# Kernel optimization log

Measured on AMD Instinct MI355X. Metric: run time of the kernel, lower is better.

## Reference

```python
import jax, jax.numpy as jnp
import numpy as np

EPS = 1e-3        # Memory.eps distance threshold
MOMENTUM = 0.999  # Memory.momentum
N, F, M = 500000, 256, 1024


def setup_inputs() -> dict:
    key = jax.random.key(0)
    k1, k2, k3, k4, k5 = jax.random.split(key, 5)
    return {
        "points": jax.random.normal(k1, (M, 3), dtype=jnp.float32),
        "descriptors": jax.random.normal(k2, (M, F), dtype=jnp.float32),
        # learned/stateful memory bank (params/buffers of the module)
        "mem_points": jax.random.normal(k3, (N, 3), dtype=jnp.float32),
        "mem_descriptors": jax.random.normal(k4, (N, F), dtype=jnp.float32),
        "usage": jax.random.randint(k5, (N,), 0, 1000, dtype=jnp.int32),
    }


def _moving(x, m):
    # faithful to Memory.moving: x*m + (1-m)*x  (== x, kept as written)
    return x * m + (1.0 - m) * x


def reference(points, descriptors, mem_points, mem_descriptors, usage):
    # ---- point_address: cdist (p=2) + argmin nearest neighbor ----
    # squared-distance expansion; [M, N] matrix
    d2 = (jnp.sum(points * points, axis=-1)[:, None]
          + jnp.sum(mem_points * mem_points, axis=-1)[None, :]
          - 2.0 * points @ mem_points.T)
    dist = jnp.sqrt(jnp.maximum(d2, 1e-12))
    dmin = jnp.min(dist, axis=-1)
    idx = jnp.argmin(dist, axis=-1)            # [M]
    mask = dmin > EPS                          # queries with no near match

    # ---- topk eviction: lowest-usage slots, assigned in query order ----
    # torch: idx[mask] = usage.topk(k=mask.sum(), largest=False).indices
    # static-shape equivalent: take top-M least-used, select first cumsum(mask)
    _, evict = jax.lax.top_k(-usage, points.shape[0])  # [M] least-used slots
    rank = jnp.cumsum(mask.astype(jnp.int32)) - 1      # position among masked
    idx = jnp.where(mask, evict[rank], idx)

    momentum = jnp.where(mask, 0.0, MOMENTUM)[:, None]  # [M, 1]

    # ---- write: usage bump + momentum scatter-update ----
    usage_new = usage.at[idx].add(1)
    pts_new = mem_points.at[idx].set(_moving(mem_points[idx], momentum))
    desc_new = mem_descriptors.at[idx].set(_moving(mem_descriptors[idx], momentum))

    out = jnp.concatenate([pts_new, desc_new], axis=1)  # [N, 3+F]
    return out, usage_new, idx
```

## Files before the change

### kernel.cpp

```cpp
#include <hip/hip_runtime.h>

#define N_TOT   500000
#define M_Q     1024
#define QB      16
#define NSPLIT  16
#define CAND_MAX 8192

#define ARGMIN_BLKS 1024
#define HIST_BLKS   32
#define USAGE_BLKS  64
#define CROWS       16
#define COPY_BLKS   (N_TOT / CROWS)
#define MEGA_BLKS   (ARGMIN_BLKS + HIST_BLKS + USAGE_BLKS + COPY_BLKS)
#define HIST_CHUNK  (N_TOT / HIST_BLKS)

static const unsigned OUT_ROWS  = 259u * (unsigned)N_TOT;
static const unsigned OUT_USAGE = OUT_ROWS;
static const unsigned OUT_IDX   = OUT_ROWS + (unsigned)N_TOT;

#define WS_PARTKEY 0
#define WS_PARTIDX 65536
#define WS_HISTP   131072
#define WS_V       262144
#define WS_CNT     262148
#define WS_KEYS    262152

__global__ __launch_bounds__(256) void k_mega(
    const float* __restrict__ pts,  const float* __restrict__ mpts,
    const float* __restrict__ mdesc, const int* __restrict__ usage,
    float* __restrict__ out,
    float* __restrict__ partKey, int* __restrict__ partIdx,
    int* __restrict__ histPart)
{
    __shared__ float smem[CROWS * 259];
    const int b   = blockIdx.x;
    const int tid = threadIdx.x;

    if (b < ARGMIN_BLKS) {
        const int qb = b & 63;
        const int ns = b >> 6;
        const int qbase = qb * QB;
        const int chunk = N_TOT / NSPLIT;
        const int n0 = ns * chunk;
        const int n1 = n0 + chunk;

        float* qs = smem;
        float* wk = smem + 64;
        int*   wi = (int*)(smem + 192);
        if (tid < QB * 3) qs[tid] = pts[qbase * 3 + tid];
        __syncthreads();

        float qx[QB], qy[QB], qz[QB];
#pragma unroll
        for (int i = 0; i < QB; i++) { qx[i] = qs[3*i]; qy[i] = qs[3*i+1]; qz[i] = qs[3*i+2]; }

        float bk[QB]; int bi[QB];
#pragma unroll
        for (int i = 0; i < QB; i++) { bk[i] = INFINITY; bi[i] = 0x7fffffff; }

        for (int n = n0 + tid; n < n1; n += 256) {
            float x = mpts[3*n+0], y = mpts[3*n+1], z = mpts[3*n+2];
            float h = 0.5f * (x*x + y*y + z*z);
#pragma unroll
            for (int i = 0; i < QB; i++) {
                float key = h - x*qx[i] - y*qy[i] - z*qz[i];
                bool lt = key < bk[i];
                bk[i] = lt ? key : bk[i];
                bi[i] = lt ? n   : bi[i];
            }
        }

        const int lane = tid & 63;
        const int wv   = tid >> 6;
#pragma unroll
        for (int off = 32; off > 0; off >>= 1) {
#pragma unroll
            for (int i = 0; i < QB; i++) {
                float ok = __shfl_down(bk[i], off, 64);
                int   oi = __shfl_down(bi[i], off, 64);
                if (ok < bk[i] || (ok == bk[i] && oi < bi[i])) { bk[i] = ok; bi[i] = oi; }
            }
        }
        if (lane == 0) {
#pragma unroll
            for (int i = 0; i < QB; i++) { wk[wv*QB + i] = bk[i]; wi[wv*QB + i] = bi[i]; }
        }
        __syncthreads();
        if (tid < QB) {
            float k = wk[tid]; int ix = wi[tid];
#pragma unroll
            for (int w = 1; w < 4; w++) {
                float ok = wk[w*QB + tid]; int oi = wi[w*QB + tid];
                if (ok < k || (ok == k && oi < ix)) { k = ok; ix = oi; }
            }
            partKey[(qbase + tid) * NSPLIT + ns] = k;
            partIdx[(qbase + tid) * NSPLIT + ns] = ix;
        }
    } else if (b < ARGMIN_BLKS + HIST_BLKS) {
        const int hb = b - ARGMIN_BLKS;
        const int r0 = hb * HIST_CHUNK;
        const int r1 = r0 + HIST_CHUNK;
        int* lh = (int*)smem;
#pragma unroll
        for (int i = 0; i < 4; i++) lh[tid + i * 256] = 0;
        __syncthreads();
        for (int n = r0 + tid; n < r1; n += 256) {
            unsigned v = (unsigned)usage[n];
            if (v > 1023u) v = 1023u;
            atomicAdd(&lh[v], 1);
        }
        __syncthreads();
#pragma unroll
        for (int i = 0; i < 4; i++) {
            int bin = tid + i * 256;
            histPart[hb * 1024 + bin] = lh[bin];
        }
    } else if (b < ARGMIN_BLKS + HIST_BLKS + USAGE_BLKS) {
        const int ub = b - ARGMIN_BLKS - HIST_BLKS;
        const int4* u4 = (const int4*)usage;
        float4* o4 = (float4*)(out + OUT_USAGE);
        const int TOT4 = N_TOT / 4;
        for (int g = ub * 256 + tid; g < TOT4; g += USAGE_BLKS * 256) {
            int4 u = u4[g];
            o4[g] = make_float4((float)u.x, (float)u.y, (float)u.z, (float)u.w);
        }
    } else {
        const int cb = b - (ARGMIN_BLKS + HIST_BLKS + USAGE_BLKS);
        const int n0 = cb * CROWS;
        const float4* src = (const float4*)(mdesc + (size_t)n0 * 256);
#pragma unroll
        for (int it = 0; it < 4; it++) {
            int g = tid + it * 256;
            float4 v = src[g];
            int e = g * 4;
            int r = e >> 8;
            int c = e & 255;
            float* d = smem + r * 259 + 3 + c;
            d[0] = v.x; d[1] = v.y; d[2] = v.z; d[3] = v.w;
        }
        if (tid < CROWS * 3) {
            int r = tid / 3, c = tid - r * 3;
            smem[r * 259 + c] = mpts[(size_t)n0 * 3 + tid];
        }
        __syncthreads();
        float4* dst4 = (float4*)(out + (size_t)cb * (CROWS * 259));
        const float4* s4 = (const float4*)smem;
#pragma unroll
        for (int it = 0; it < 5; it++) {
            int g = tid + it * 256;
            if (g < CROWS * 259 / 4) dst4[g] = s4[g];
        }
    }
}

__global__ __launch_bounds__(1024) void k_scanV(
    const int* __restrict__ histPart, int* __restrict__ Vout, int* __restrict__ cnt)
{
    __shared__ int scan[1024];
    const int t = threadIdx.x;
    int h = 0;
#pragma unroll
    for (int b = 0; b < HIST_BLKS; b++) h += histPart[b * 1024 + t];
    scan[t] = h; __syncthreads();
    for (int off = 1; off < 1024; off <<= 1) {
        int add = (t >= off) ? scan[t - off] : 0;
        __syncthreads();
        scan[t] += add;
        __syncthreads();
    }
    int cum  = scan[t] - h;
    int cumN = scan[t];
    if (cum < M_Q && cumN >= M_Q) { *Vout = t; *cnt = 0; }
}

__global__ __launch_bounds__(256) void k_collect(
    const int* __restrict__ usage, const int* __restrict__ Vp,
    int* __restrict__ cnt, unsigned* __restrict__ keys)
{
    const int V = *Vp;
    const int stride = gridDim.x * 256;
    for (int n = blockIdx.x * 256 + threadIdx.x; n < N_TOT; n += stride) {
        int u = usage[n];
        if (u <= V) {
            int p = atomicAdd(cnt, 1);
            if (p < CAND_MAX) keys[p] = ((unsigned)u << 19) | (unsigned)n;
        }
    }
}

__global__ __launch_bounds__(1024) void k_final(
    const float* __restrict__ pts,
    const float* __restrict__ partKey, const int* __restrict__ partIdx,
    const int* __restrict__ cntP, const unsigned* __restrict__ keysG,
    float* __restrict__ out)
{
    __shared__ unsigned keys[CAND_MAX];
    __shared__ int      mscan[1024];
    const int t = threadIdx.x;

    float bk = INFINITY; int bi = 0x7fffffff;
#pragma unroll
    for (int s = 0; s < NSPLIT; s++) {
        float k = partKey[t * NSPLIT + s];
        int   i = partIdx[t * NSPLIT + s];
        if (k < bk) { bk = k; bi = i; }
    }
    float px = pts[3*t], py = pts[3*t+1], pz = pts[3*t+2];
    float d2 = px*px + py*py + pz*pz + 2.0f * bk;
    const bool mask = d2 > 1e-6f;

    int C = *cntP; if (C > CAND_MAX) C = CAND_MAX;
    int P2 = 1; while (P2 < C) P2 <<= 1;
    for (int p = t; p < P2; p += 1024) keys[p] = (p < C) ? keysG[p] : 0xFFFFFFFFu;
    __syncthreads();

    for (int k = 2; k <= P2; k <<= 1) {
        for (int j = k >> 1; j > 0; j >>= 1) {
            for (int i = t; i < P2; i += 1024) {
                int ixj = i ^ j;
                if (ixj > i) {
                    unsigned a = keys[i], bb = keys[ixj];
                    bool up = ((i & k) == 0);
                    if ((a > bb) == up) { keys[i] = bb; keys[ixj] = a; }
                }
            }
            __syncthreads();
        }
    }

    mscan[t] = mask ? 1 : 0; __syncthreads();
    for (int off = 1; off < 1024; off <<= 1) {
        int add = (t >= off) ? mscan[t - off] : 0;
        __syncthreads();
        mscan[t] += add;
        __syncthreads();
    }
    int rank = mscan[t] - 1;
    int idx = mask ? (int)(keys[rank] & 0x7FFFFu) : bi;
    out[(size_t)OUT_IDX + (size_t)t] = (float)idx;
    atomicAdd(out + OUT_USAGE + idx, 1.0f);
}

extern "C" void kernel_launch(void* const* d_in, const int* in_sizes, int n_in,
                              void* d_out, int out_size, void* d_ws, size_t ws_size,
                              hipStream_t stream)
{
    (void)in_sizes; (void)n_in; (void)out_size; (void)ws_size;
    const float* pts   = (const float*)d_in[0];
    const float* mpts  = (const float*)d_in[2];
    const float* mdesc = (const float*)d_in[3];
    const int*   usage = (const int*)d_in[4];
    float* out = (float*)d_out;

    char* ws = (char*)d_ws;
    float*    partKey  = (float*)(ws + WS_PARTKEY);
    int*      partIdx  = (int*)(ws + WS_PARTIDX);
    int*      histPart = (int*)(ws + WS_HISTP);
    int*      Vp       = (int*)(ws + WS_V);
    int*      cnt      = (int*)(ws + WS_CNT);
    unsigned* keys     = (unsigned*)(ws + WS_KEYS);

    k_mega<<<MEGA_BLKS, 256, 0, stream>>>(pts, mpts, mdesc, usage, out,
                                          partKey, partIdx, histPart);
    k_scanV<<<1, 1024, 0, stream>>>(histPart, Vp, cnt);
    k_collect<<<64, 256, 0, stream>>>(usage, Vp, cnt, keys);
    k_final<<<1, 1024, 0, stream>>>(pts, partKey, partIdx, cnt, keys, out);
}
```

Measured before the change: 331.7 us.

## Split fused mega-kernel into separate argmin, histogram, usage and copy kernels

Breaks the heterogeneous block-dispatched mega kernel into dedicated kernels for argmin, usage histogram, usage conversion and row copy. The bulk descriptor copy now runs last, after the final index kernel. The aim is to give each phase its own shared-memory footprint and launch shape; argmin blocks no longer reserve the copy's 16 KB of shared memory. The trade-off is that the compute-bound argmin and the bandwidth-bound copy no longer run concurrently on one stream, and there are more launches.

New measurement: 386.3 us. 16.5% more time.

```diff
diff --git a/kernel.cpp b/kernel.cpp
--- a/kernel.cpp
+++ b/kernel.cpp
@@ -11,7 +11,6 @@
 #define USAGE_BLKS  64
 #define CROWS       16
 #define COPY_BLKS   (N_TOT / CROWS)
-#define MEGA_BLKS   (ARGMIN_BLKS + HIST_BLKS + USAGE_BLKS + COPY_BLKS)
 #define HIST_CHUNK  (N_TOT / HIST_BLKS)
 
 static const unsigned OUT_ROWS  = 259u * (unsigned)N_TOT;
@@ -25,131 +24,94 @@
 #define WS_CNT     262148
 #define WS_KEYS    262152
 
-__global__ __launch_bounds__(256) void k_mega(
-    const float* __restrict__ pts,  const float* __restrict__ mpts,
-    const float* __restrict__ mdesc, const int* __restrict__ usage,
-    float* __restrict__ out,
-    float* __restrict__ partKey, int* __restrict__ partIdx,
-    int* __restrict__ histPart)
-{
-    __shared__ float smem[CROWS * 259];
-    const int b   = blockIdx.x;
+__global__ __launch_bounds__(256) void k_argmin(
+    const float* __restrict__ pts, const float* __restrict__ mpts,
+    float* __restrict__ partKey, int* __restrict__ partIdx)
+{
+    const int b = blockIdx.x;
+    const int qb = b & 63;
+    const int ns = b >> 6;
+    const int qbase = qb * QB;
+    const int chunk = N_TOT / NSPLIT;
+    const int n0 = ns * chunk;
+    const int n1 = n0 + chunk;
+
+    __shared__ float qs[QB * 3];
+    __shared__ float wk[4][QB];
+    __shared__ int   wi[4][QB];
     const int tid = threadIdx.x;
-
-    if (b < ARGMIN_BLKS) {
-        const int qb = b & 63;
-        const int ns = b >> 6;
-        const int qbase = qb * QB;
-        const int chunk = N_TOT / NSPLIT;
-        const int n0 = ns * chunk;
-        const int n1 = n0 + chunk;
-
-        float* qs = smem;
-        float* wk = smem + 64;
-        int*   wi = (int*)(smem + 192);
-        if (tid < QB * 3) qs[tid] = pts[qbase * 3 + tid];
-        __syncthreads();
-
-        float qx[QB], qy[QB], qz[QB];
-#pragma unroll
-        for (int i = 0; i < QB; i++) { qx[i] = qs[3*i]; qy[i] = qs[3*i+1]; qz[i] = qs[3*i+2]; }
-
-        float bk[QB]; int bi[QB];
-#pragma unroll
-        for (int i = 0; i < QB; i++) { bk[i] = INFINITY; bi[i] = 0x7fffffff; }
-
-        for (int n = n0 + tid; n < n1; n += 256) {
-            float x = mpts[3*n+0], y = mpts[3*n+1], z = mpts[3*n+2];
-            float h = 0.5f * (x*x + y*y + z*z);
-#pragma unroll
-            for (int i = 0; i < QB; i++) {
-                float key = h - x*qx[i] - y*qy[i] - z*qz[i];
-                bool lt = key < bk[i];
-                bk[i] = lt ? key : bk[i];
-                bi[i] = lt ? n   : bi[i];
-            }
-        }
-
-        const int lane = tid & 63;
-        const int wv   = tid >> 6;
-#pragma unroll
-        for (int off = 32; off > 0; off >>= 1) {
-#pragma unroll
-            for (int i = 0; i < QB; i++) {
-                float ok = __shfl_down(bk[i], off, 64);
-                int   oi = __shfl_down(bi[i], off, 64);
-                if (ok < bk[i] || (ok == bk[i] && oi < bi[i])) { bk[i] = ok; bi[i] = oi; }
-            }
-        }
-        if (lane == 0) {
-#pragma unroll
-            for (int i = 0; i < QB; i++) { wk[wv*QB + i] = bk[i]; wi[wv*QB + i] = bi[i]; }
-        }
-        __syncthreads();
-        if (tid < QB) {
-            float k = wk[tid]; int ix = wi[tid];
-#pragma unroll
-            for (int w = 1; w < 4; w++) {
-                float ok = wk[w*QB + tid]; int oi = wi[w*QB + tid];
-                if (ok < k || (ok == k && oi < ix)) { k = ok; ix = oi; }
-            }
-            partKey[(qbase + tid) * NSPLIT + ns] = k;
-            partIdx[(qbase + tid) * NSPLIT + ns] = ix;
-        }
-    } else if (b < ARGMIN_BLKS + HIST_BLKS) {
-        const int hb = b - ARGMIN_BLKS;
-        const int r0 = hb * HIST_CHUNK;
-        const int r1 = r0 + HIST_CHUNK;
-        int* lh = (int*)smem;
-#pragma unroll
-        for (int i = 0; i < 4; i++) lh[tid + i * 256] = 0;
-        __syncthreads();
-        for (int n = r0 + tid; n < r1; n += 256) {
-            unsigned v = (unsigned)usage[n];
-            if (v > 1023u) v = 1023u;
-            atomicAdd(&lh[v], 1);
-        }
-        __syncthreads();
-#pragma unroll
-        for (int i = 0; i < 4; i++) {
-            int bin = tid + i * 256;
-            histPart[hb * 1024 + bin] = lh[bin];
-        }
-    } else if (b < ARGMIN_BLKS + HIST_BLKS + USAGE_BLKS) {
-        const int ub = b - ARGMIN_BLKS - HIST_BLKS;
-        const int4* u4 = (const int4*)usage;
-        float4* o4 = (float4*)(out + OUT_USAGE);
-        const int TOT4 = N_TOT / 4;
-        for (int g = ub * 256 + tid; g < TOT4; g += USAGE_BLKS * 256) {
-            int4 u = u4[g];
-            o4[g] = make_float4((float)u.x, (float)u.y, (float)u.z, (float)u.w);
-        }
-    } else {
-        const int cb = b - (ARGMIN_BLKS + HIST_BLKS + USAGE_BLKS);
-        const int n0 = cb * CROWS;
-        const float4* src = (const float4*)(mdesc + (size_t)n0 * 256);
-#pragma unroll
-        for (int it = 0; it < 4; it++) {
-            int g = tid + it * 256;
-            float4 v = src[g];
-            int e = g * 4;
-            int r = e >> 8;
-            int c = e & 255;
-            float* d = smem + r * 259 + 3 + c;
-            d[0] = v.x; d[1] = v.y; d[2] = v.z; d[3] = v.w;
-        }
-        if (tid < CROWS * 3) {
-            int r = tid / 3, c = tid - r * 3;
-            smem[r * 259 + c] = mpts[(size_t)n0 * 3 + tid];
-        }
-        __syncthreads();
-        float4* dst4 = (float4*)(out + (size_t)cb * (CROWS * 259));
-        const float4* s4 = (const float4*)smem;
-#pragma unroll
-        for (int it = 0; it < 5; it++) {
-            int g = tid + it * 256;
-            if (g < CROWS * 259 / 4) dst4[g] = s4[g];
-        }
+    if (tid < QB * 3) qs[tid] = pts[qbase * 3 + tid];
+    __syncthreads();
+
+    float qx[QB], qy[QB], qz[QB];
+#pragma unroll
+    for (int i = 0; i < QB; i++) { qx[i] = qs[3*i]; qy[i] = qs[3*i+1]; qz[i] = qs[3*i+2]; }
+
+    float bk[QB]; int bi[QB];
+#pragma unroll
+    for (int i = 0; i < QB; i++) { bk[i] = INFINITY; bi[i] = 0x7fffffff; }
+
+    for (int n = n0 + tid; n < n1; n += 256) {
+        float x = mpts[3*n+0], y = mpts[3*n+1], z = mpts[3*n+2];
+        float h = 0.5f * (x*x + y*y + z*z);
+#pragma unroll
+        for (int i = 0; i < QB; i++) {
+            float key = h - x*qx[i] - y*qy[i] - z*qz[i];
+            bool lt = key < bk[i];
+            bk[i] = lt ? key : bk[i];
+            bi[i] = lt ? n   : bi[i];
+        }
+    }
+
+    const int lane = tid & 63;
+    const int wv   = tid >> 6;
+#pragma unroll
+    for (int off = 32; off > 0; off >>= 1) {
+#pragma unroll
+        for (int i = 0; i < QB; i++) {
+            float ok = __shfl_down(bk[i], off, 64);
+            int   oi = __shfl_down(bi[i], off, 64);
+            if (ok < bk[i] || (ok == bk[i] && oi < bi[i])) { bk[i] = ok; bi[i] = oi; }
+        }
+    }
+    if (lane == 0) {
+#pragma unroll
+        for (int i = 0; i < QB; i++) { wk[wv][i] = bk[i]; wi[wv][i] = bi[i]; }
+    }
+    __syncthreads();
+    if (tid < QB) {
+        float k = wk[0][tid]; int ix = wi[0][tid];
+#pragma unroll
+        for (int w = 1; w < 4; w++) {
+            float ok = wk[w][tid]; int oi = wi[w][tid];
+            if (ok < k || (ok == k && oi < ix)) { k = ok; ix = oi; }
+        }
+        partKey[(qbase + tid) * NSPLIT + ns] = k;
+        partIdx[(qbase + tid) * NSPLIT + ns] = ix;
+    }
+}
+
+__global__ __launch_bounds__(256) void k_hist(
+    const int* __restrict__ usage, int* __restrict__ histPart)
+{
+    __shared__ int lh[1024];
+    const int hb = blockIdx.x;
+    const int tid = threadIdx.x;
+    const int r0 = hb * HIST_CHUNK;
+    const int r1 = r0 + HIST_CHUNK;
+#pragma unroll
+    for (int i = 0; i < 4; i++) lh[tid + i * 256] = 0;
+    __syncthreads();
+    for (int n = r0 + tid; n < r1; n += 256) {
+        unsigned v = (unsigned)usage[n];
+        if (v > 1023u) v = 1023u;
+        atomicAdd(&lh[v], 1);
+    }
+    __syncthreads();
+#pragma unroll
+    for (int i = 0; i < 4; i++) {
+        int bin = tid + i * 256;
+        histPart[hb * 1024 + bin] = lh[bin];
     }
 }
 
@@ -185,6 +147,19 @@
             int p = atomicAdd(cnt, 1);
             if (p < CAND_MAX) keys[p] = ((unsigned)u << 19) | (unsigned)n;
         }
+    }
+}
+
+__global__ __launch_bounds__(256) void k_usage(
+    const int* __restrict__ usage, float* __restrict__ out)
+{
+    const int4* u4 = (const int4*)usage;
+    float4* o4 = (float4*)(out + OUT_USAGE);
+    const int TOT4 = N_TOT / 4;
+    const int stride = gridDim.x * 256;
+    for (int g = blockIdx.x * 256 + threadIdx.x; g < TOT4; g += stride) {
+        int4 u = u4[g];
+        o4[g] = make_float4((float)u.x, (float)u.y, (float)u.z, (float)u.w);
     }
 }
 
@@ -241,6 +216,41 @@
     atomicAdd(out + OUT_USAGE + idx, 1.0f);
 }
 
+__global__ __launch_bounds__(256) void k_copy(
+    const float* __restrict__ mpts, const float* __restrict__ mdesc,
+    float* __restrict__ out)
+{
+    __shared__ float smem[CROWS * 259];
+    const int cb  = blockIdx.x;
+    const int tid = threadIdx.x;
+    const int n0  = cb * CROWS;
+
+    const float4* src = (const float4*)(mdesc + (size_t)n0 * 256);
+#pragma unroll
+    for (int it = 0; it < 4; it++) {
+        int g = tid + it * 256;
+        float4 v = src[g];
+        int e = g * 4;
+        int r = e >> 8;
+        int c = e & 255;
+        float* d = smem + r * 259 + 3 + c;
+        d[0] = v.x; d[1] = v.y; d[2] = v.z; d[3] = v.w;
+    }
+    if (tid < CROWS * 3) {
+        int r = tid / 3, c = tid - r * 3;
+        smem[r * 259 + c] = mpts[(size_t)n0 * 3 + tid];
+    }
+    __syncthreads();
+
+    float4* dst4 = (float4*)(out + (size_t)cb * (CROWS * 259));
+    const float4* s4 = (const float4*)smem;
+#pragma unroll
+    for (int it = 0; it < 5; it++) {
+        int g = tid + it * 256;
+        if (g < CROWS * 259 / 4) dst4[g] = s4[g];
+    }
+}
+
 extern "C" void kernel_launch(void* const* d_in, const int* in_sizes, int n_in,
                               void* d_out, int out_size, void* d_ws, size_t ws_size,
                               hipStream_t stream)
@@ -260,9 +270,11 @@
     int*      cnt      = (int*)(ws + WS_CNT);
     unsigned* keys     = (unsigned*)(ws + WS_KEYS);
 
-    k_mega<<<MEGA_BLKS, 256, 0, stream>>>(pts, mpts, mdesc, usage, out,
-                                          partKey, partIdx, histPart);
+    k_argmin<<<ARGMIN_BLKS, 256, 0, stream>>>(pts, mpts, partKey, partIdx);
+    k_hist<<<HIST_BLKS, 256, 0, stream>>>(usage, histPart);
     k_scanV<<<1, 1024, 0, stream>>>(histPart, Vp, cnt);
     k_collect<<<64, 256, 0, stream>>>(usage, Vp, cnt, keys);
+    k_usage<<<USAGE_BLKS, 256, 0, stream>>>(usage, out);
     k_final<<<1, 1024, 0, stream>>>(pts, partKey, partIdx, cnt, keys, out);
-}
+    k_copy<<<COPY_BLKS, 256, 0, stream>>>(mpts, mdesc, out);
+}
```

## Fuse threshold scan and candidate collection into final kernel; drop LDS staging in copy

Applied to the files above, without the earlier changes.

The histogram prefix scan and the low-usage candidate collection move into the single-block final kernel. Candidates now go into shared memory through a shared atomic counter, which removes two kernel launches and the global workspace round trip. The cost is that one block of 1024 threads must now read the whole usage array serially. The descriptor copy path now writes float4s straight to the 259-stride output rows instead of staging them in LDS. This drops a barrier and cuts the shared-memory footprint, but the stores become misaligned (offset by 3 floats).

Result: slower. 386.9 us (+16.6%).

```diff
diff --git a/kernel.cpp b/kernel.cpp
--- a/kernel.cpp
+++ b/kernel.cpp
@@ -21,9 +21,6 @@
 #define WS_PARTKEY 0
 #define WS_PARTIDX 65536
 #define WS_HISTP   131072
-#define WS_V       262144
-#define WS_CNT     262148
-#define WS_KEYS    262152
 
 __global__ __launch_bounds__(256) void k_mega(
     const float* __restrict__ pts,  const float* __restrict__ mpts,
@@ -32,7 +29,7 @@
     float* __restrict__ partKey, int* __restrict__ partIdx,
     int* __restrict__ histPart)
 {
-    __shared__ float smem[CROWS * 259];
+    __shared__ int smem[1024];
     const int b   = blockIdx.x;
     const int tid = threadIdx.x;
 
@@ -44,9 +41,9 @@
         const int n0 = ns * chunk;
         const int n1 = n0 + chunk;
 
-        float* qs = smem;
-        float* wk = smem + 64;
-        int*   wi = (int*)(smem + 192);
+        float* qs = (float*)smem;
+        float* wk = (float*)smem + 64;
+        int*   wi = smem + 192;
         if (tid < QB * 3) qs[tid] = pts[qbase * 3 + tid];
         __syncthreads();
 
@@ -100,20 +97,19 @@
         const int hb = b - ARGMIN_BLKS;
         const int r0 = hb * HIST_CHUNK;
         const int r1 = r0 + HIST_CHUNK;
-        int* lh = (int*)smem;
-#pragma unroll
-        for (int i = 0; i < 4; i++) lh[tid + i * 256] = 0;
+#pragma unroll
+        for (int i = 0; i < 4; i++) smem[tid + i * 256] = 0;
         __syncthreads();
         for (int n = r0 + tid; n < r1; n += 256) {
             unsigned v = (unsigned)usage[n];
             if (v > 1023u) v = 1023u;
-            atomicAdd(&lh[v], 1);
+            atomicAdd(&smem[v], 1);
         }
         __syncthreads();
 #pragma unroll
         for (int i = 0; i < 4; i++) {
             int bin = tid + i * 256;
-            histPart[hb * 1024 + bin] = lh[bin];
+            histPart[hb * 1024 + bin] = smem[bin];
         }
     } else if (b < ARGMIN_BLKS + HIST_BLKS + USAGE_BLKS) {
         const int ub = b - ARGMIN_BLKS - HIST_BLKS;
@@ -128,74 +124,30 @@
         const int cb = b - (ARGMIN_BLKS + HIST_BLKS + USAGE_BLKS);
         const int n0 = cb * CROWS;
         const float4* src = (const float4*)(mdesc + (size_t)n0 * 256);
+        float* obase = out + (size_t)n0 * 259;
 #pragma unroll
         for (int it = 0; it < 4; it++) {
             int g = tid + it * 256;
             float4 v = src[g];
-            int e = g * 4;
-            int r = e >> 8;
-            int c = e & 255;
-            float* d = smem + r * 259 + 3 + c;
-            d[0] = v.x; d[1] = v.y; d[2] = v.z; d[3] = v.w;
+            int r = g >> 6;
+            int c = (g & 63) << 2;
+            *reinterpret_cast<float4*>(obase + r * 259 + 3 + c) = v;
         }
         if (tid < CROWS * 3) {
             int r = tid / 3, c = tid - r * 3;
-            smem[r * 259 + c] = mpts[(size_t)n0 * 3 + tid];
-        }
-        __syncthreads();
-        float4* dst4 = (float4*)(out + (size_t)cb * (CROWS * 259));
-        const float4* s4 = (const float4*)smem;
-#pragma unroll
-        for (int it = 0; it < 5; it++) {
-            int g = tid + it * 256;
-            if (g < CROWS * 259 / 4) dst4[g] = s4[g];
+            obase[r * 259 + c] = mpts[(size_t)n0 * 3 + tid];
         }
     }
 }
 
-__global__ __launch_bounds__(1024) void k_scanV(
-    const int* __restrict__ histPart, int* __restrict__ Vout, int* __restrict__ cnt)
+__global__ __launch_bounds__(1024) void k_final(
+    const float* __restrict__ pts, const int* __restrict__ usage,
+    const float* __restrict__ partKey, const int* __restrict__ partIdx,
+    const int* __restrict__ histPart, float* __restrict__ out)
 {
-    __shared__ int scan[1024];
-    const int t = threadIdx.x;
-    int h = 0;
-#pragma unroll
-    for (int b = 0; b < HIST_BLKS; b++) h += histPart[b * 1024 + t];
-    scan[t] = h; __syncthreads();
-    for (int off = 1; off < 1024; off <<= 1) {
-        int add = (t >= off) ? scan[t - off] : 0;
-        __syncthreads();
-        scan[t] += add;
-        __syncthreads();
-    }
-    int cum  = scan[t] - h;
-    int cumN = scan[t];
-    if (cum < M_Q && cumN >= M_Q) { *Vout = t; *cnt = 0; }
-}
-
-__global__ __launch_bounds__(256) void k_collect(
-    const int* __restrict__ usage, const int* __restrict__ Vp,
-    int* __restrict__ cnt, unsigned* __restrict__ keys)
-{
-    const int V = *Vp;
-    const int stride = gridDim.x * 256;
-    for (int n = blockIdx.x * 256 + threadIdx.x; n < N_TOT; n += stride) {
-        int u = usage[n];
-        if (u <= V) {
-            int p = atomicAdd(cnt, 1);
-            if (p < CAND_MAX) keys[p] = ((unsigned)u << 19) | (unsigned)n;
-        }
-    }
-}
-
-__global__ __launch_bounds__(1024) void k_final(
-    const float* __restrict__ pts,
-    const float* __restrict__ partKey, const int* __restrict__ partIdx,
-    const int* __restrict__ cntP, const unsigned* __restrict__ keysG,
-    float* __restrict__ out)
-{
+    __shared__ int      scan[1024];
     __shared__ unsigned keys[CAND_MAX];
-    __shared__ int      mscan[1024];
+    __shared__ int      s_cnt, s_V;
     const int t = threadIdx.x;
 
     float bk = INFINITY; int bi = 0x7fffffff;
@@ -209,9 +161,42 @@
     float d2 = px*px + py*py + pz*pz + 2.0f * bk;
     const bool mask = d2 > 1e-6f;
 
-    int C = *cntP; if (C > CAND_MAX) C = CAND_MAX;
+    int h = 0;
+#pragma unroll
+    for (int b = 0; b < HIST_BLKS; b++) h += histPart[b * 1024 + t];
+    scan[t] = h;
+    if (t == 0) s_cnt = 0;
+    __syncthreads();
+    for (int off = 1; off < 1024; off <<= 1) {
+        int add = (t >= off) ? scan[t - off] : 0;
+        __syncthreads();
+        scan[t] += add;
+        __syncthreads();
+    }
+    int cum  = scan[t] - h;
+    int cumN = scan[t];
+    if (cum < M_Q && cumN >= M_Q) s_V = t;
+    __syncthreads();
+    const int V = s_V;
+
+    const int4* u4 = (const int4*)usage;
+    const int TOT4 = N_TOT / 4;
+    for (int g = t; g < TOT4; g += 1024) {
+        int4 u = u4[g];
+        int n = g * 4;
+#pragma unroll
+        for (int j = 0; j < 4; j++) {
+            int uv = (j == 0) ? u.x : (j == 1) ? u.y : (j == 2) ? u.z : u.w;
+            if (uv <= V) {
+                int p = atomicAdd(&s_cnt, 1);
+                if (p < CAND_MAX) keys[p] = ((unsigned)uv << 19) | (unsigned)(n + j);
+            }
+        }
+    }
+    __syncthreads();
+    int C = s_cnt; if (C > CAND_MAX) C = CAND_MAX;
     int P2 = 1; while (P2 < C) P2 <<= 1;
-    for (int p = t; p < P2; p += 1024) keys[p] = (p < C) ? keysG[p] : 0xFFFFFFFFu;
+    for (int p = C + t; p < P2; p += 1024) keys[p] = 0xFFFFFFFFu;
     __syncthreads();
 
     for (int k = 2; k <= P2; k <<= 1) {
@@ -228,14 +213,14 @@
         }
     }
 
-    mscan[t] = mask ? 1 : 0; __syncthreads();
+    scan[t] = mask ? 1 : 0; __syncthreads();
     for (int off = 1; off < 1024; off <<= 1) {
-        int add = (t >= off) ? mscan[t - off] : 0;
-        __syncthreads();
-        mscan[t] += add;
-        __syncthreads();
-    }
-    int rank = mscan[t] - 1;
+        int add = (t >= off) ? scan[t - off] : 0;
+        __syncthreads();
+        scan[t] += add;
+        __syncthreads();
+    }
+    int rank = scan[t] - 1;
     int idx = mask ? (int)(keys[rank] & 0x7FFFFu) : bi;
     out[(size_t)OUT_IDX + (size_t)t] = (float)idx;
     atomicAdd(out + OUT_USAGE + idx, 1.0f);
@@ -253,16 +238,11 @@
     float* out = (float*)d_out;
 
     char* ws = (char*)d_ws;
-    float*    partKey  = (float*)(ws + WS_PARTKEY);
-    int*      partIdx  = (int*)(ws + WS_PARTIDX);
-    int*      histPart = (int*)(ws + WS_HISTP);
-    int*      Vp       = (int*)(ws + WS_V);
-    int*      cnt      = (int*)(ws + WS_CNT);
-    unsigned* keys     = (unsigned*)(ws + WS_KEYS);
+    float* partKey  = (float*)(ws + WS_PARTKEY);
+    int*   partIdx  = (int*)(ws + WS_PARTIDX);
+    int*   histPart = (int*)(ws + WS_HISTP);
 
     k_mega<<<MEGA_BLKS, 256, 0, stream>>>(pts, mpts, mdesc, usage, out,
                                           partKey, partIdx, histPart);
-    k_scanV<<<1, 1024, 0, stream>>>(histPart, Vp, cnt);
-    k_collect<<<64, 256, 0, stream>>>(usage, Vp, cnt, keys);
-    k_final<<<1, 1024, 0, stream>>>(pts, partKey, partIdx, cnt, keys, out);
+    k_final<<<1, 1024, 0, stream>>>(pts, usage, partKey, partIdx, histPart, out);
 }
```

## Split descriptor copy into flat grid-stride kernel and separate points-scatter kernel

Applied to the files above, without the earlier changes.

The LDS-staged 16-row copy blocks are removed from the fused mega kernel. A standalone grid-stride kernel now copies descriptors straight to the output rows using float4 stores at offset 259*n+3+c. A second small kernel scatters the 3 point coordinates per row. The aim is to drop the shared-memory staging and the barrier per copy block. In exchange, the float4 stores are misaligned, the point columns touch the same cache lines a second time, and the copy no longer overlaps with the argmin work because the kernels run one after another.

Result: slower. 462.4 us (+39.4%).

```diff
diff --git a/kernel.cpp b/kernel.cpp
--- a/kernel.cpp
+++ b/kernel.cpp
@@ -9,10 +9,11 @@
 #define ARGMIN_BLKS 1024
 #define HIST_BLKS   32
 #define USAGE_BLKS  64
-#define CROWS       16
-#define COPY_BLKS   (N_TOT / CROWS)
-#define MEGA_BLKS   (ARGMIN_BLKS + HIST_BLKS + USAGE_BLKS + COPY_BLKS)
+#define SMALL_BLKS  (ARGMIN_BLKS + HIST_BLKS + USAGE_BLKS)
 #define HIST_CHUNK  (N_TOT / HIST_BLKS)
+
+#define COPY_GRID   2048
+#define MPTS_GRID   512
 
 static const unsigned OUT_ROWS  = 259u * (unsigned)N_TOT;
 static const unsigned OUT_USAGE = OUT_ROWS;
@@ -25,14 +26,41 @@
 #define WS_CNT     262148
 #define WS_KEYS    262152
 
-__global__ __launch_bounds__(256) void k_mega(
+__global__ __launch_bounds__(256) void k_copy_flat(
+    const float* __restrict__ mdesc, float* __restrict__ out)
+{
+    const unsigned TOT4 = (unsigned)N_TOT * 64u;
+    const unsigned stride = COPY_GRID * 256u;
+    unsigned g0 = blockIdx.x * 256u + threadIdx.x;
+#pragma unroll 4
+    for (unsigned g = g0; g < TOT4; g += stride) {
+        float4 v = *reinterpret_cast<const float4*>(mdesc + (size_t)g * 4u);
+        unsigned n = g >> 6;
+        unsigned c = (g & 63u) << 2;
+        *reinterpret_cast<float4*>(out + (size_t)n * 259u + 3u + c) = v;
+    }
+}
+
+__global__ __launch_bounds__(256) void k_mpts(
+    const float* __restrict__ mpts, float* __restrict__ out)
+{
+    const int TOT = N_TOT * 3;
+    const int stride = MPTS_GRID * 256;
+    for (int g = blockIdx.x * 256 + threadIdx.x; g < TOT; g += stride) {
+        int n = g / 3;
+        int r = g - n * 3;
+        out[(size_t)n * 259u + r] = mpts[g];
+    }
+}
+
+__global__ __launch_bounds__(256) void k_small(
     const float* __restrict__ pts,  const float* __restrict__ mpts,
-    const float* __restrict__ mdesc, const int* __restrict__ usage,
+    const int* __restrict__ usage,
     float* __restrict__ out,
     float* __restrict__ partKey, int* __restrict__ partIdx,
     int* __restrict__ histPart)
 {
-    __shared__ float smem[CROWS * 259];
+    __shared__ int smem[1024];
     const int b   = blockIdx.x;
     const int tid = threadIdx.x;
 
@@ -44,9 +72,9 @@
         const int n0 = ns * chunk;
         const int n1 = n0 + chunk;
 
-        float* qs = smem;
-        float* wk = smem + 64;
-        int*   wi = (int*)(smem + 192);
+        float* qs = (float*)smem;
+        float* wk = (float*)smem + 64;
+        int*   wi = smem + 192;
         if (tid < QB * 3) qs[tid] = pts[qbase * 3 + tid];
         __syncthreads();
 
@@ -100,22 +128,21 @@
         const int hb = b - ARGMIN_BLKS;
         const int r0 = hb * HIST_CHUNK;
         const int r1 = r0 + HIST_CHUNK;
-        int* lh = (int*)smem;
-#pragma unroll
-        for (int i = 0; i < 4; i++) lh[tid + i * 256] = 0;
+#pragma unroll
+        for (int i = 0; i < 4; i++) smem[tid + i * 256] = 0;
         __syncthreads();
         for (int n = r0 + tid; n < r1; n += 256) {
             unsigned v = (unsigned)usage[n];
             if (v > 1023u) v = 1023u;
-            atomicAdd(&lh[v], 1);
+            atomicAdd(&smem[v], 1);
         }
         __syncthreads();
 #pragma unroll
         for (int i = 0; i < 4; i++) {
             int bin = tid + i * 256;
-            histPart[hb * 1024 + bin] = lh[bin];
-        }
-    } else if (b < ARGMIN_BLKS + HIST_BLKS + USAGE_BLKS) {
+            histPart[hb * 1024 + bin] = smem[bin];
+        }
+    } else {
         const int ub = b - ARGMIN_BLKS - HIST_BLKS;
         const int4* u4 = (const int4*)usage;
         float4* o4 = (float4*)(out + OUT_USAGE);
@@ -123,32 +150,6 @@
         for (int g = ub * 256 + tid; g < TOT4; g += USAGE_BLKS * 256) {
             int4 u = u4[g];
             o4[g] = make_float4((float)u.x, (float)u.y, (float)u.z, (float)u.w);
-        }
-    } else {
-        const int cb = b - (ARGMIN_BLKS + HIST_BLKS + USAGE_BLKS);
-        const int n0 = cb * CROWS;
-        const float4* src = (const float4*)(mdesc + (size_t)n0 * 256);
-#pragma unroll
-        for (int it = 0; it < 4; it++) {
-            int g = tid + it * 256;
-            float4 v = src[g];
-            int e = g * 4;
-            int r = e >> 8;
-            int c = e & 255;
-            float* d = smem + r * 259 + 3 + c;
-            d[0] = v.x; d[1] = v.y; d[2] = v.z; d[3] = v.w;
-        }
-        if (tid < CROWS * 3) {
-            int r = tid / 3, c = tid - r * 3;
-            smem[r * 259 + c] = mpts[(size_t)n0 * 3 + tid];
-        }
-        __syncthreads();
-        float4* dst4 = (float4*)(out + (size_t)cb * (CROWS * 259));
-        const float4* s4 = (const float4*)smem;
-#pragma unroll
-        for (int it = 0; it < 5; it++) {
-            int g = tid + it * 256;
-            if (g < CROWS * 259 / 4) dst4[g] = s4[g];
         }
     }
 }
@@ -260,8 +261,10 @@
     int*      cnt      = (int*)(ws + WS_CNT);
     unsigned* keys     = (unsigned*)(ws + WS_KEYS);
 
-    k_mega<<<MEGA_BLKS, 256, 0, stream>>>(pts, mpts, mdesc, usage, out,
-                                          partKey, partIdx, histPart);
+    k_copy_flat<<<COPY_GRID, 256, 0, stream>>>(mdesc, out);
+    k_mpts<<<MPTS_GRID, 256, 0, stream>>>(mpts, out);
+    k_small<<<SMALL_BLKS, 256, 0, stream>>>(pts, mpts, usage, out,
+                                            partKey, partIdx, histPart);
     k_scanV<<<1, 1024, 0, stream>>>(histPart, Vp, cnt);
     k_collect<<<64, 256, 0, stream>>>(usage, Vp, cnt, keys);
     k_final<<<1, 1024, 0, stream>>>(pts, partKey, partIdx, cnt, keys, out);
```
